# Kernel tuning notes

Measured on AMD Instinct MI355X. Metric: run time of the kernel, lower is better.

The kernel has to match this reference:

```python
import jax, jax.numpy as jnp
import numpy as np

N_NODES = 100000
N_EDGES = 1600000
IN_F = 64
OUT_F = 32
NEG_SLOPE = 0.2


def setup_inputs() -> dict:
    key = jax.random.key(0)
    k = jax.random.split(key, 6)
    x = jax.random.normal(k[0], (N_NODES, IN_F), dtype=jnp.float32)
    edge_index = jax.random.randint(k[1], (2, N_EDGES), 0, N_NODES, dtype=jnp.int64)
    W = jax.random.normal(k[2], (IN_F, OUT_F), dtype=jnp.float32) * 0.1
    att_src = jax.random.normal(k[3], (OUT_F,), dtype=jnp.float32) * 0.1
    att_dst = jax.random.normal(k[4], (OUT_F,), dtype=jnp.float32) * 0.1
    bias = jax.random.normal(k[5], (OUT_F,), dtype=jnp.float32) * 0.1
    return {"x": x, "edge_index": edge_index, "W": W,
            "att_src": att_src, "att_dst": att_dst, "bias": bias}


def reference(x, edge_index, W, att_src, att_dst, bias):
    N = x.shape[0]
    # Linear projection (single head, concat=True -> [N, OUT_F])
    h = x @ W  # [N, C]
    a_src = h @ att_src  # [N] per-node source attention logit contribution
    a_dst = h @ att_dst  # [N] per-node destination contribution
    # add self loops (PyG GATConv default add_self_loops=True)
    loop = jnp.arange(N, dtype=edge_index.dtype)
    src = jnp.concatenate([edge_index[0], loop])  # [E+N] message senders
    dst = jnp.concatenate([edge_index[1], loop])  # [E+N] message receivers
    # attention logits per edge, LeakyReLU(alpha_src[j] + alpha_dst[i])
    e = jax.nn.leaky_relu(a_src[src] + a_dst[dst], NEG_SLOPE)
    # segment softmax over incoming edges of each destination node
    m = jax.ops.segment_max(e, dst, num_segments=N)  # every node has a self loop
    ex = jnp.exp(e - m[dst])
    denom = jax.ops.segment_sum(ex, dst, num_segments=N)
    alpha = ex / denom[dst]  # [E+N]
    # weighted scatter-add of source features into destinations
    out = jax.ops.segment_sum(h[src] * alpha[:, None], dst, num_segments=N)
    out = out + bias
    # GATLayer activation='relu'
    return jax.nn.relu(out)
```

## Files before the change

### kernel.cpp

```cpp
#include <hip/hip_runtime.h>
#include <hip/hip_fp16.h>
#include <math.h>

#define IN_F 64
#define OUT_F 32
#define NEG_SLOPE 0.2f

#define BK_SHIFT 7
#define BK 128
#define NBMAX 1024
#define NBLKA 256
#define PSTAGE 5
#define COLCAP 4096

typedef _Float16 half8_t __attribute__((ext_vector_type(8)));
typedef float float4_t __attribute__((ext_vector_type(4)));
typedef int int4_t __attribute__((ext_vector_type(4)));


__device__ __forceinline__ float leaky(float v) {
    return (v > 0.0f) ? v : NEG_SLOPE * v;
}

__device__ __forceinline__ int incScan256(int v, int tid, int* wsum) {
    const int lane = tid & 63, wid = tid >> 6;
    #pragma unroll
    for (int m = 1; m < 64; m <<= 1) {
        int u = __shfl_up(v, m);
        if (lane >= m) v += u;
    }
    if (lane == 63) wsum[wid] = v;
    __syncthreads();
    int add = 0;
    for (int k = 0; k < wid; ++k) add += wsum[k];
    __syncthreads();
    return v + add;
}

__device__ __forceinline__ int incScan512(int v, int tid, int* wsum) {
    const int lane = tid & 63, wid = tid >> 6;
    #pragma unroll
    for (int m = 1; m < 64; m <<= 1) {
        int u = __shfl_up(v, m);
        if (lane >= m) v += u;
    }
    if (lane == 63) wsum[wid] = v;
    __syncthreads();
    int add = 0;
    for (int k = 0; k < wid; ++k) add += wsum[k];
    __syncthreads();
    return v + add;
}

__global__ __launch_bounds__(256) void k_projhist(
        const float* __restrict__ x, const float* __restrict__ W,
        const float* __restrict__ att_src, const float* __restrict__ att_dst,
        __half2* __restrict__ h2, float* __restrict__ asrc, float* __restrict__ adst,
        const int* __restrict__ dst, int* __restrict__ hist,
        int N, int NB, int E, int epb, int PB) {
    __shared__ int smem[2560];
    const int tid = threadIdx.x;

    if (blockIdx.x >= PB) {
        int* lh = smem;
        const int blk = blockIdx.x - PB;
        for (int i = tid; i < NB; i += 256) lh[i] = 0;
        __syncthreads();
        const int e0 = blk * epb, e1 = min(E, e0 + epb);
        for (int e = e0 + tid; e < e1; e += 256) atomicAdd(&lh[dst[e] >> BK_SHIFT], 1);
        __syncthreads();
        for (int b = tid; b < NB; b += 256) hist[(size_t)b * NBLKA + blk] = lh[b];
        return;
    }

    const int wv   = tid >> 6;
    const int lane = tid & 63;
    const int m    = lane & 15;
    const int quad = lane >> 4;
    const int node0 = (blockIdx.x * 4 + wv) * 16;
    if (node0 >= N) return;

    const int kb = quad * 8;
    half8_t b00, b01, b10, b11;
    #pragma unroll
    for (int j = 0; j < 8; ++j) {
        b00[j] = (_Float16)W[(kb + j) * OUT_F + m];
        b01[j] = (_Float16)W[(32 + kb + j) * OUT_F + m];
        b10[j] = (_Float16)W[(kb + j) * OUT_F + 16 + m];
        b11[j] = (_Float16)W[(32 + kb + j) * OUT_F + 16 + m];
    }
    const int row = min(node0 + m, N - 1);
    const float* xr = x + (size_t)row * IN_F + kb;
    float4_t xa = *(const float4_t*)(xr);
    float4_t xb = *(const float4_t*)(xr + 4);
    float4_t xc = *(const float4_t*)(xr + 32);
    float4_t xd = *(const float4_t*)(xr + 36);
    half8_t a0, a1;
    #pragma unroll
    for (int j = 0; j < 4; ++j) {
        a0[j] = (_Float16)xa[j]; a0[4 + j] = (_Float16)xb[j];
        a1[j] = (_Float16)xc[j]; a1[4 + j] = (_Float16)xd[j];
    }
    float4_t acc0 = {0.f, 0.f, 0.f, 0.f};
    float4_t acc1 = {0.f, 0.f, 0.f, 0.f};
    acc0 = __builtin_amdgcn_mfma_f32_16x16x32_f16(a0, b00, acc0, 0, 0, 0);
    acc0 = __builtin_amdgcn_mfma_f32_16x16x32_f16(a1, b01, acc0, 0, 0, 0);
    acc1 = __builtin_amdgcn_mfma_f32_16x16x32_f16(a0, b10, acc1, 0, 0, 0);
    acc1 = __builtin_amdgcn_mfma_f32_16x16x32_f16(a1, b11, acc1, 0, 0, 0);

    const float aS0 = att_src[m], aS1 = att_src[16 + m];
    const float aD0 = att_dst[m], aD1 = att_dst[16 + m];
    #pragma unroll
    for (int r = 0; r < 4; ++r) {
        const int node = node0 + quad * 4 + r;
        float h0 = acc0[r], h1 = acc1[r];
        float h0p = __shfl_xor(h0, 1);
        float h1p = __shfl_xor(h1, 1);
        if (node < N && (m & 1) == 0) {
            __half2 hv;
            hv.x = __float2half_rn(h0); hv.y = __float2half_rn(h0p);
            h2[(size_t)node * 16 + (m >> 1)] = hv;
            __half2 hw;
            hw.x = __float2half_rn(h1); hw.y = __float2half_rn(h1p);
            h2[(size_t)node * 16 + 8 + (m >> 1)] = hw;
        }
        float vs = h0 * aS0 + h1 * aS1;
        float vd = h0 * aD0 + h1 * aD1;
        #pragma unroll
        for (int mm = 1; mm < 16; mm <<= 1) {
            vs += __shfl_xor(vs, mm);
            vd += __shfl_xor(vd, mm);
        }
        if (node < N && m == 0) {
            asrc[node] = vs;
            adst[node] = vd;
        }
    }
}

__global__ __launch_bounds__(256) void k_scan1(int* __restrict__ hist,
                                               int* __restrict__ bsum,
                                               __half2* __restrict__ h2,
                                               float* __restrict__ asrc,
                                               int N, int NB) {
    __shared__ int wsum[4];
    const int b = blockIdx.x, tid = threadIdx.x;
    if (b == 0) {
        if (tid < 16) h2[(size_t)N * 16 + tid] = __floats2half2_rn(0.0f, 0.0f);
        if (tid == 16) asrc[N] = -1e30f;
    }
    int v = hist[(size_t)b * NBLKA + tid];
    const int inc = incScan256(v, tid, wsum);
    hist[(size_t)b * NBLKA + tid] = inc - v;
    if (tid == 255) bsum[b] = inc;
}

__global__ __launch_bounds__(512) void k_bpart(const int* __restrict__ src,
                                               const int* __restrict__ dst,
                                               const int* __restrict__ hist,
                                               const int* __restrict__ bsum,
                                               int* __restrict__ recs,
                                               int NB, int E, int epb) {
    __shared__ int tt[NBMAX];
    __shared__ int lcur[NBMAX];
    __shared__ int wsum[8];
    const int tid = threadIdx.x, blk = blockIdx.x;
    for (int i = tid; i < NBMAX; i += 512) tt[i] = (i < NB) ? bsum[i] : 0;
    __syncthreads();
    {
        int a0 = tt[tid * 2], a1 = tt[tid * 2 + 1];
        int s = a0 + a1;
        int inc = incScan512(s, tid, wsum);
        int run = inc - s;
        tt[tid * 2] = run; run += a0;
        tt[tid * 2 + 1] = run;
    }
    __syncthreads();
    for (int b = tid; b < NB; b += 512)
        lcur[b] = hist[(size_t)b * NBLKA + blk] + tt[b];
    __syncthreads();
    const int e0 = blk * epb, e1 = min(E, e0 + epb);
    for (int e = e0 + tid; e < e1; e += 512) {
        int s = src[e];
        int d = dst[e];
        int p = atomicAdd(&lcur[d >> BK_SHIFT], 1);
        recs[p] = ((d & (BK - 1)) << 17) | s;
    }
}

__global__ __launch_bounds__(512) void k_pg(const int* __restrict__ recs,
                                            const int* __restrict__ bsum,
                                            const float* __restrict__ asrc,
                                            const float* __restrict__ adst,
                                            const __half2* __restrict__ h2,
                                            const float* __restrict__ bias,
                                            float* __restrict__ out,
                                            int NB, int E, int N) {
    __shared__ int tt[NBMAX];
    __shared__ __align__(16) int colsh[COLCAP];
    __shared__ int fineCnt[BK];
    __shared__ int cur[BK];
    __shared__ int loff[BK];
    __shared__ int lpad[BK];
    __shared__ int wsum[8];
    const int b = blockIdx.x, tid = threadIdx.x;
    const int node0 = b << BK_SHIFT;

    for (int i = tid; i < NBMAX; i += 512) tt[i] = (i < NB) ? bsum[i] : 0;
    __syncthreads();
    {
        int a0 = tt[tid * 2], a1 = tt[tid * 2 + 1];
        int s = a0 + a1;
        int inc = incScan512(s, tid, wsum);
        int run = inc - s;
        tt[tid * 2] = run;
        tt[tid * 2 + 1] = run + a0;
    }
    __syncthreads();
    const int cb0 = tt[b];
    const int cb1 = (b + 1 < NB) ? tt[b + 1] : E;
    const int count = cb1 - cb0;

    for (int i = tid; i < COLCAP; i += 512) colsh[i] = N;
    if (tid < BK) fineCnt[tid] = 0;
    __syncthreads();

    int myrec[PSTAGE];
    #pragma unroll
    for (int k = 0; k < PSTAGE; ++k) {
        int i = tid + k * 512;
        if (i < count) {
            int v = recs[cb0 + i];
            myrec[k] = v;
            atomicAdd(&fineCnt[v >> 17], 1);
        }
    }
    for (int i = tid + PSTAGE * 512; i < count; i += 512)
        atomicAdd(&fineCnt[recs[cb0 + i] >> 17], 1);
    __syncthreads();

    const int v0 = (tid < BK) ? fineCnt[tid] : 0;
    const int pv = (v0 + 3) & ~3;
    const int vin = (tid < BK) ? pv : 0;
    const int pinc = incScan512(vin, tid, wsum);
    const int pexcl = pinc - vin;
    if (tid < BK) {
        loff[tid] = pexcl;
        lpad[tid] = pv;
        cur[tid]  = pexcl;
    }
    __syncthreads();

    #pragma unroll
    for (int k = 0; k < PSTAGE; ++k) {
        int i = tid + k * 512;
        if (i < count) {
            int r = myrec[k];
            int p = atomicAdd(&cur[r >> 17], 1);
            colsh[p] = r & 0x1FFFF;
        }
    }
    for (int i = tid + PSTAGE * 512; i < count; i += 512) {
        int r = recs[cb0 + i];
        int p = atomicAdd(&cur[r >> 17], 1);
        colsh[p] = r & 0x1FFFF;
    }
    __syncthreads();

    const int wid  = tid >> 6;
    const int lane = tid & 63;
    const int g    = lane >> 4;
    const int c2   = lane & 15;
    for (int i = 0; i < 16; ++i) {
        const int dloc = wid * 16 + i;
        const int n = node0 + dloc;
        if (n >= N) break;
        const float adst_n = adst[n];
        float l = 0.0f, accx = 0.0f, accy = 0.0f;
        if (g == 0) {
            float p = __expf(leaky(asrc[n] + adst_n));
            float2 hv = __half22float2(h2[(size_t)n * 16 + c2]);
            l = p; accx = p * hv.x; accy = p * hv.y;
        }
        const int base = loff[dloc];
        const int nch  = lpad[dloc] >> 2;
        for (int c = g; c < nch; c += 4) {
            const int4_t cc = *(const int4_t*)(&colsh[base + c * 4]);
            const int s0 = cc[0], s1 = cc[1], s2 = cc[2], s3 = cc[3];
            float a0 = asrc[s0], a1 = asrc[s1], a2 = asrc[s2], a3 = asrc[s3];
            float2 h0 = __half22float2(h2[(size_t)s0 * 16 + c2]);
            float2 h1 = __half22float2(h2[(size_t)s1 * 16 + c2]);
            float2 hv2 = __half22float2(h2[(size_t)s2 * 16 + c2]);
            float2 h3 = __half22float2(h2[(size_t)s3 * 16 + c2]);
            float p0 = __expf(leaky(a0 + adst_n));
            float p1 = __expf(leaky(a1 + adst_n));
            float p2 = __expf(leaky(a2 + adst_n));
            float p3 = __expf(leaky(a3 + adst_n));
            l += (p0 + p1) + (p2 + p3);
            accx += p0 * h0.x + p1 * h1.x + p2 * hv2.x + p3 * h3.x;
            accy += p0 * h0.y + p1 * h1.y + p2 * hv2.y + p3 * h3.y;
        }
        l    += __shfl_xor(l, 16);    l    += __shfl_xor(l, 32);
        accx += __shfl_xor(accx, 16); accx += __shfl_xor(accx, 32);
        accy += __shfl_xor(accy, 16); accy += __shfl_xor(accy, 32);
        if (g == 0) {
            float inv = 1.0f / l;
            float2 bb = ((const float2*)bias)[c2];
            float2 o;
            o.x = fmaxf(accx * inv + bb.x, 0.0f);
            o.y = fmaxf(accy * inv + bb.y, 0.0f);
            ((float2*)out)[(size_t)n * 16 + c2] = o;
        }
    }
}

extern "C" void kernel_launch(void* const* d_in, const int* in_sizes, int n_in,
                              void* d_out, int out_size, void* d_ws, size_t ws_size,
                              hipStream_t stream) {
    const float* x        = (const float*)d_in[0];
    const int*   eidx     = (const int*)d_in[1];
    const float* W        = (const float*)d_in[2];
    const float* att_src  = (const float*)d_in[3];
    const float* att_dst  = (const float*)d_in[4];
    const float* bias     = (const float*)d_in[5];
    float* out = (float*)d_out;

    const int N = in_sizes[0] / IN_F;
    const int E = in_sizes[1] / 2;
    const int* src = eidx;
    const int* dst = eidx + E;

    const int NB  = (N + BK - 1) >> BK_SHIFT;
    const int epb = (E + NBLKA - 1) / NBLKA;

    int* u = (int*)d_ws;
    size_t o = 0;
    __half2* h2   = (__half2*)(u + o); o += (size_t)(N + 1) * 16;
    float*   asrc = (float*)(u + o);   o += N + 1;
    float*   adst = (float*)(u + o);   o += N;
    int*     hist = u + o;             o += (size_t)NB * NBLKA;
    int*     bsum = u + o;             o += NBMAX;
    int*     recs = u + o;             o += E;

    const int PB = (N + 63) / 64;

    k_projhist<<<PB + NBLKA, 256, 0, stream>>>(x, W, att_src, att_dst, h2, asrc, adst,
                                               dst, hist, N, NB, E, epb, PB);
    k_scan1<<<NB, 256, 0, stream>>>(hist, bsum, h2, asrc, N, NB);
    k_bpart<<<NBLKA, 512, 0, stream>>>(src, dst, hist, bsum, recs, NB, E, epb);
    k_pg<<<NB, 512, 0, stream>>>(recs, bsum, asrc, adst, h2, bias, out, NB, E, N);
}
```

Before: 158.5 us.

## Halve destination bucket size and compute bucket offsets once in partition kernel

```diff
diff --git a/kernel.cpp b/kernel.cpp
--- a/kernel.cpp
+++ b/kernel.cpp
@@ -6,12 +6,12 @@
 #define OUT_F 32
 #define NEG_SLOPE 0.2f
 
-#define BK_SHIFT 7
-#define BK 128
-#define NBMAX 1024
+#define BK_SHIFT 6
+#define BK 64
+#define NBMAX 2048
 #define NBLKA 256
-#define PSTAGE 5
-#define COLCAP 4096
+#define PSTAGE 3
+#define COLCAP 2048
 
 typedef _Float16 half8_t __attribute__((ext_vector_type(8)));
 typedef float float4_t __attribute__((ext_vector_type(4)));
@@ -160,6 +160,7 @@
                                                const int* __restrict__ hist,
                                                const int* __restrict__ bsum,
                                                int* __restrict__ recs,
+                                               int* __restrict__ boff,
                                                int NB, int E, int epb) {
     __shared__ int tt[NBMAX];
     __shared__ int lcur[NBMAX];
@@ -168,14 +169,20 @@
     for (int i = tid; i < NBMAX; i += 512) tt[i] = (i < NB) ? bsum[i] : 0;
     __syncthreads();
     {
-        int a0 = tt[tid * 2], a1 = tt[tid * 2 + 1];
-        int s = a0 + a1;
+        int a0 = tt[tid * 4], a1 = tt[tid * 4 + 1], a2 = tt[tid * 4 + 2], a3 = tt[tid * 4 + 3];
+        int s = a0 + a1 + a2 + a3;
         int inc = incScan512(s, tid, wsum);
         int run = inc - s;
-        tt[tid * 2] = run; run += a0;
-        tt[tid * 2 + 1] = run;
-    }
-    __syncthreads();
+        tt[tid * 4] = run;     run += a0;
+        tt[tid * 4 + 1] = run; run += a1;
+        tt[tid * 4 + 2] = run; run += a2;
+        tt[tid * 4 + 3] = run;
+    }
+    __syncthreads();
+    if (blk == 0) {
+        for (int b = tid; b < NB; b += 512) boff[b] = tt[b];
+        if (tid == 0) boff[NB] = E;
+    }
     for (int b = tid; b < NB; b += 512)
         lcur[b] = hist[(size_t)b * NBLKA + blk] + tt[b];
     __syncthreads();
@@ -189,14 +196,13 @@
 }
 
 __global__ __launch_bounds__(512) void k_pg(const int* __restrict__ recs,
-                                            const int* __restrict__ bsum,
+                                            const int* __restrict__ boff,
                                             const float* __restrict__ asrc,
                                             const float* __restrict__ adst,
                                             const __half2* __restrict__ h2,
                                             const float* __restrict__ bias,
                                             float* __restrict__ out,
                                             int NB, int E, int N) {
-    __shared__ int tt[NBMAX];
     __shared__ __align__(16) int colsh[COLCAP];
     __shared__ int fineCnt[BK];
     __shared__ int cur[BK];
@@ -206,19 +212,8 @@
     const int b = blockIdx.x, tid = threadIdx.x;
     const int node0 = b << BK_SHIFT;
 
-    for (int i = tid; i < NBMAX; i += 512) tt[i] = (i < NB) ? bsum[i] : 0;
-    __syncthreads();
-    {
-        int a0 = tt[tid * 2], a1 = tt[tid * 2 + 1];
-        int s = a0 + a1;
-        int inc = incScan512(s, tid, wsum);
-        int run = inc - s;
-        tt[tid * 2] = run;
-        tt[tid * 2 + 1] = run + a0;
-    }
-    __syncthreads();
-    const int cb0 = tt[b];
-    const int cb1 = (b + 1 < NB) ? tt[b + 1] : E;
+    const int cb0 = boff[b];
+    const int cb1 = boff[b + 1];
     const int count = cb1 - cb0;
 
     for (int i = tid; i < COLCAP; i += 512) colsh[i] = N;
@@ -271,8 +266,8 @@
     const int lane = tid & 63;
     const int g    = lane >> 4;
     const int c2   = lane & 15;
-    for (int i = 0; i < 16; ++i) {
-        const int dloc = wid * 16 + i;
+    for (int i = 0; i < 8; ++i) {
+        const int dloc = wid * 8 + i;
         const int n = node0 + dloc;
         if (n >= N) break;
         const float adst_n = adst[n];
@@ -340,6 +335,7 @@
     float*   adst = (float*)(u + o);   o += N;
     int*     hist = u + o;             o += (size_t)NB * NBLKA;
     int*     bsum = u + o;             o += NBMAX;
+    int*     boff = u + o;             o += NBMAX + 1;
     int*     recs = u + o;             o += E;
 
     const int PB = (N + 63) / 64;
@@ -347,6 +343,6 @@
     k_projhist<<<PB + NBLKA, 256, 0, stream>>>(x, W, att_src, att_dst, h2, asrc, adst,
                                                dst, hist, N, NB, E, epb, PB);
     k_scan1<<<NB, 256, 0, stream>>>(hist, bsum, h2, asrc, N, NB);
-    k_bpart<<<NBLKA, 512, 0, stream>>>(src, dst, hist, bsum, recs, NB, E, epb);
-    k_pg<<<NB, 512, 0, stream>>>(recs, bsum, asrc, adst, h2, bias, out, NB, E, N);
-}
+    k_bpart<<<NBLKA, 512, 0, stream>>>(src, dst, hist, bsum, recs, boff, NB, E, epb);
+    k_pg<<<NB, 512, 0, stream>>>(recs, boff, asrc, adst, h2, bias, out, NB, E, N);
+}
```

Measured after the change: 158.7 us. Within noise of the previous version (+0.1%).
